# Optimization experiments

Measured on AMD Instinct MI355X. Metric: run time of the kernel, lower is better.

Reference implementation:

```python
import jax, jax.numpy as jnp
import numpy as np

N_NODES = 100000


def gcn_conv(x, edge_index, W, b):
    """PyG-style GCNConv: symmetric-normalized A+I propagation of x @ W, plus bias."""
    n = x.shape[0]
    src, dst = edge_index[0], edge_index[1]
    loops = jnp.arange(n, dtype=src.dtype)
    src = jnp.concatenate([src, loops])  # add self loops
    dst = jnp.concatenate([dst, loops])
    deg = jax.ops.segment_sum(jnp.ones_like(src, dtype=x.dtype), dst, num_segments=n)
    dinv = jnp.where(deg > 0, jax.lax.rsqrt(deg), 0.0)
    norm = dinv[src] * dinv[dst]  # [E+n]
    h = x @ W  # [n, out]
    msg = h[src] * norm[:, None]  # gather + scale
    out = jax.ops.segment_sum(msg, dst, num_segments=n)  # scatter-add
    return out + b


def setup_inputs() -> dict:
    key = jax.random.key(0)
    ks = jax.random.split(key, 5)
    x = jax.random.normal(ks[0], (N_NODES, 4), dtype=jnp.float32)
    edge_index = jax.random.randint(ks[1], (2, 3200000), 0, N_NODES, dtype=jnp.int64)
    W1 = jax.random.normal(ks[2], (4, 64), dtype=jnp.float32) * 0.5
    b1 = jnp.zeros((64,), dtype=jnp.float32)
    W2 = jax.random.normal(ks[3], (64, 32), dtype=jnp.float32) * 0.125
    b2 = jnp.zeros((32,), dtype=jnp.float32)
    return {"x": x, "edge_index": edge_index, "W1": W1, "b1": b1, "W2": W2, "b2": b2}


def reference(x, edge_index, W1, b1, W2, b2):
    h = gcn_conv(x, edge_index, W1, b1)
    h = jax.nn.relu(h)
    # F.dropout with training=False is identity (eval-mode reference)
    h = gcn_conv(h, edge_index, W2, b2)
    return jnp.mean(h, axis=0)  # [32]
```

## Files before the change

### kernel.cpp

```cpp
#include <hip/hip_runtime.h>

#define ST 512
#define EPB 8192
#define HT 1024
#define FT 1024
#define S_LOG 8
#define S 256
#define CAP 8912
#define MAXB 512

__device__ __forceinline__ void gAtomAdd(float* p, float v) {
    unsafeAtomicAdd(p, v);
}

__global__ void k_init(int* __restrict__ cur_d, int* __restrict__ cur_s,
                       float* __restrict__ g, int nb) {
    int t = threadIdx.x;
    if (t < nb) { cur_d[t] = t * CAP; cur_s[t] = t * CAP; }
    if (t < 64) g[t] = 0.0f;
}

__global__ void __launch_bounds__(ST) k_sctr2(
        const int4* __restrict__ src4, const int4* __restrict__ dst4, int E,
        int* __restrict__ cur_d, int* __restrict__ cur_s,
        unsigned* __restrict__ rec_d, unsigned* __restrict__ rec_s, int nb) {
    __shared__ unsigned lrec[EPB];
    __shared__ unsigned short lbkt[EPB];
    __shared__ int cnt[MAXB];
    __shared__ int lst[MAXB];
    __shared__ int gb[MAXB];
    __shared__ int wsum[8];
    int t = threadIdx.x;
    int lane = t & 63, wv = t >> 6;
    int E4 = E >> 2;
    int b4 = blockIdx.x * (EPB / 4);
    int m = min(EPB, E - blockIdx.x * EPB);

    int4 dk[4], sk[4];
    bool v[4];
    #pragma unroll
    for (int k = 0; k < 4; ++k) {
        int idx = b4 + k * ST + t;
        v[k] = idx < E4;
        if (v[k]) { dk[k] = dst4[idx]; sk[k] = src4[idx]; }
    }

    for (int ph = 0; ph < 2; ++ph) {
        int* cursor = ph ? cur_s : cur_d;
        unsigned* rec = ph ? rec_s : rec_d;
        cnt[t] = 0;
        __syncthreads();
        int rk[16];
        #pragma unroll
        for (int k = 0; k < 4; ++k) {
            if (v[k]) {
                int4 K = ph ? sk[k] : dk[k];
                rk[4 * k + 0] = atomicAdd(&cnt[K.x >> S_LOG], 1);
                rk[4 * k + 1] = atomicAdd(&cnt[K.y >> S_LOG], 1);
                rk[4 * k + 2] = atomicAdd(&cnt[K.z >> S_LOG], 1);
                rk[4 * k + 3] = atomicAdd(&cnt[K.w >> S_LOG], 1);
            }
        }
        __syncthreads();
        int c = cnt[t];
        int ic = c;
        #pragma unroll
        for (int o = 1; o < 64; o <<= 1) {
            int u = __shfl_up(ic, o);
            if (lane >= o) ic += u;
        }
        if (lane == 63) wsum[wv] = ic;
        __syncthreads();
        int pre = 0;
        #pragma unroll
        for (int k = 0; k < 7; ++k) pre += (k < wv) ? wsum[k] : 0;
        ic += pre;
        lst[t] = ic - c;
        gb[t] = (c > 0) ? atomicAdd(&cursor[t], c) : 0;
        __syncthreads();
        #pragma unroll
        for (int k = 0; k < 4; ++k) {
            if (v[k]) {
                int4 K = ph ? sk[k] : dk[k];
                int4 P = ph ? dk[k] : sk[k];
                int bb, p;
                bb = K.x >> S_LOG; p = lst[bb] + rk[4 * k + 0];
                lrec[p] = ((unsigned)P.x << S_LOG) | (unsigned)(K.x & (S - 1));
                lbkt[p] = (unsigned short)bb;
                bb = K.y >> S_LOG; p = lst[bb] + rk[4 * k + 1];
                lrec[p] = ((unsigned)P.y << S_LOG) | (unsigned)(K.y & (S - 1));
                lbkt[p] = (unsigned short)bb;
                bb = K.z >> S_LOG; p = lst[bb] + rk[4 * k + 2];
                lrec[p] = ((unsigned)P.z << S_LOG) | (unsigned)(K.z & (S - 1));
                lbkt[p] = (unsigned short)bb;
                bb = K.w >> S_LOG; p = lst[bb] + rk[4 * k + 3];
                lrec[p] = ((unsigned)P.w << S_LOG) | (unsigned)(K.w & (S - 1));
                lbkt[p] = (unsigned short)bb;
            }
        }
        __syncthreads();
        for (int i = t; i < m; i += ST) {
            int bb = lbkt[i];
            rec[gb[bb] + (i - lst[bb])] = lrec[i];
        }
        __syncthreads();
    }
}

__global__ void __launch_bounds__(HT) k_hist(
        const unsigned* __restrict__ rec_d, const int* __restrict__ cur_d,
        const float4* __restrict__ x, float* __restrict__ dinv,
        float4* __restrict__ y, int n) {
    __shared__ int cnt[S];
    int b = blockIdx.x, t = threadIdx.x;
    if (t < S) cnt[t] = 0;
    __syncthreads();
    int lo = b * CAP;
    int m = cur_d[b] - lo;
    int m4 = m >> 2;
    const uint4* rec4 = (const uint4*)(rec_d + lo);
    for (int i = t; i < m4; i += HT) {
        uint4 r = rec4[i];
        atomicAdd(&cnt[r.x & (S - 1)], 1);
        atomicAdd(&cnt[r.y & (S - 1)], 1);
        atomicAdd(&cnt[r.z & (S - 1)], 1);
        atomicAdd(&cnt[r.w & (S - 1)], 1);
    }
    for (int i = (m4 << 2) + t; i < m; i += HT)
        atomicAdd(&cnt[rec_d[lo + i] & (S - 1)], 1);
    __syncthreads();
    int nd = (b << S_LOG) + t;
    if (t < S && nd < n) {
        float dv = rsqrtf((float)cnt[t] + 1.0f);
        dinv[nd] = dv;
        float4 xi = x[nd];
        y[nd] = make_float4(dv * xi.x, dv * xi.y, dv * xi.z, dv * xi.w);
    }
}

__global__ void __launch_bounds__(FT) k_fuse(
        const unsigned* __restrict__ rec_d, const unsigned* __restrict__ rec_s,
        const int* __restrict__ cur_d, const int* __restrict__ cur_s,
        const float4* __restrict__ y, const float* __restrict__ dinv,
        const float* __restrict__ W1, const float* __restrict__ b1,
        float* __restrict__ g, int n) {
    __shared__ unsigned lrec[CAP];
    __shared__ int cnt[S];
    __shared__ int nst[S];
    __shared__ float a[S];
    __shared__ float4 lp1[S];
    __shared__ float red[FT];
    __shared__ int wsum[4];
    int b = blockIdx.x, t = threadIdx.x;
    int lane = t & 63, wv = t >> 6;
    if (t < S) { cnt[t] = 0; a[t] = 0.0f; }
    __syncthreads();
    int lo = b * CAP;
    int md = cur_d[b] - lo;
    unsigned rv[9]; int rr[9];
    #pragma unroll
    for (int k = 0; k < 9; ++k) {
        int i = t + k * FT;
        if (i < md) {
            unsigned r = rec_d[lo + i];
            rv[k] = r;
            rr[k] = atomicAdd(&cnt[r & (S - 1)], 1);
        }
    }
    __syncthreads();
    int c = 0, ic = 0;
    if (t < S) {
        c = cnt[t]; ic = c;
        #pragma unroll
        for (int o = 1; o < 64; o <<= 1) {
            int u = __shfl_up(ic, o);
            if (lane >= o) ic += u;
        }
        if (lane == 63) wsum[wv] = ic;
    }
    __syncthreads();
    if (t < S) {
        int pre = 0;
        #pragma unroll
        for (int k = 0; k < 3; ++k) pre += (k < wv) ? wsum[k] : 0;
        ic += pre;
        cnt[t] = ic;
        nst[t] = ic - c;
    }
    __syncthreads();
    #pragma unroll
    for (int k = 0; k < 9; ++k) {
        int i = t + k * FT;
        if (i < md) lrec[nst[rv[k] & (S - 1)] + rr[k]] = rv[k] >> S_LOG;
    }
    int ms = cur_s[b] - lo;
    int ms4 = ms >> 2;
    const uint4* rs4 = (const uint4*)(rec_s + lo);
    for (int i = t; i < ms4; i += FT) {
        uint4 r = rs4[i];
        float d0 = dinv[r.x >> S_LOG], d1 = dinv[r.y >> S_LOG];
        float d2 = dinv[r.z >> S_LOG], d3 = dinv[r.w >> S_LOG];
        atomicAdd(&a[r.x & (S - 1)], d0);
        atomicAdd(&a[r.y & (S - 1)], d1);
        atomicAdd(&a[r.z & (S - 1)], d2);
        atomicAdd(&a[r.w & (S - 1)], d3);
    }
    for (int i = (ms4 << 2) + t; i < ms; i += FT) {
        unsigned r = rec_s[lo + i];
        atomicAdd(&a[r & (S - 1)], dinv[r >> S_LOG]);
    }
    __syncthreads();
    int node = t >> 2, q = t & 3;
    int nd = (b << S_LOG) + node;
    if (nd < n) {
        int j1 = cnt[node];
        int j = nst[node] + q;
        float a0 = 0.0f, a1 = 0.0f, a2 = 0.0f, a3 = 0.0f;
        for (; j + 12 < j1; j += 16) {
            int s0 = lrec[j], s1 = lrec[j + 4], s2 = lrec[j + 8], s3 = lrec[j + 12];
            float4 y0 = y[s0], y1 = y[s1], y2 = y[s2], y3 = y[s3];
            a0 += y0.x + y1.x + y2.x + y3.x;
            a1 += y0.y + y1.y + y2.y + y3.y;
            a2 += y0.z + y1.z + y2.z + y3.z;
            a3 += y0.w + y1.w + y2.w + y3.w;
        }
        for (; j < j1; j += 4) {
            float4 ys = y[lrec[j]];
            a0 += ys.x; a1 += ys.y; a2 += ys.z; a3 += ys.w;
        }
        a0 += __shfl_down(a0, 2); a1 += __shfl_down(a1, 2);
        a2 += __shfl_down(a2, 2); a3 += __shfl_down(a3, 2);
        a0 += __shfl_down(a0, 1); a1 += __shfl_down(a1, 1);
        a2 += __shfl_down(a2, 1); a3 += __shfl_down(a3, 1);
        if (q == 0) {
            float di = dinv[nd];
            lp1[node] = make_float4(di * a0, di * a1, di * a2, di * a3);
        }
    }
    __syncthreads();
    int cch = t & 63, w = t >> 6;
    float w0 = W1[cch], w1 = W1[64 + cch], w2 = W1[128 + cch], w3 = W1[192 + cch];
    float bb = b1[cch];
    int nb0 = b << S_LOG;
    float facc = 0.0f;
    for (int k = w; k < S; k += 16) {
        int ndk = nb0 + k;
        if (ndk >= n) break;
        float di = dinv[ndk];
        float4 p = lp1[k];
        float4 yi = y[ndk];
        float h0 = fmaf(di, yi.x, p.x);
        float h1 = fmaf(di, yi.y, p.y);
        float h2 = fmaf(di, yi.z, p.z);
        float h3 = fmaf(di, yi.w, p.w);
        float h = fmaf(h0, w0, fmaf(h1, w1, fmaf(h2, w2, fmaf(h3, w3, bb))));
        h = fmaxf(h, 0.0f);
        float wi = fmaf(di, a[k], di * di);
        facc = fmaf(wi, h, facc);
    }
    red[t] = facc;
    __syncthreads();
    if (t < 64) {
        float s = red[t];
        #pragma unroll
        for (int o = 1; o < 16; ++o) s += red[t + 64 * o];
        gAtomAdd(&g[t], s);
    }
}

__global__ void k_final(const float* __restrict__ g, const float* __restrict__ W2,
                        const float* __restrict__ b2, float* __restrict__ out, float inv_n) {
    int j = threadIdx.x;
    if (j < 32) {
        float a = 0.0f;
        #pragma unroll
        for (int c = 0; c < 64; ++c) a = fmaf(g[c], W2[c * 32 + j], a);
        out[j] = fmaf(a, inv_n, b2[j]);
    }
}

extern "C" void kernel_launch(void* const* d_in, const int* in_sizes, int n_in,
                              void* d_out, int out_size, void* d_ws, size_t ws_size,
                              hipStream_t stream) {
    const float* x  = (const float*)d_in[0];
    const int*   ei = (const int*)d_in[1];
    const float* W1 = (const float*)d_in[2];
    const float* b1 = (const float*)d_in[3];
    const float* W2 = (const float*)d_in[4];
    const float* b2 = (const float*)d_in[5];
    float* out = (float*)d_out;

    int n = in_sizes[0] / 4;
    int E = in_sizes[1] / 2;
    const int* src = ei;
    const int* dst = ei + E;
    int NB = (n + S - 1) >> S_LOG;

    char* ws = (char*)d_ws;
    int* cur_d = (int*)ws;
    int* cur_s = cur_d + 512;
    float* g   = (float*)(cur_s + 512);
    size_t ctrl = 1600;
    unsigned* rec_d = (unsigned*)ws + ctrl;
    unsigned* rec_s = rec_d + (size_t)NB * CAP;
    float* y    = (float*)(rec_s + (size_t)NB * CAP);
    float* dinv = y + 4 * (size_t)n;

    int NSB = (E + EPB - 1) / EPB;

    k_init<<<1, 512, 0, stream>>>(cur_d, cur_s, g, NB);
    k_sctr2<<<NSB, ST, 0, stream>>>((const int4*)src, (const int4*)dst, E,
                                    cur_d, cur_s, rec_d, rec_s, NB);
    k_hist<<<NB, HT, 0, stream>>>(rec_d, cur_d, (const float4*)x, dinv,
                                  (float4*)y, n);
    k_fuse<<<NB, FT, 0, stream>>>(rec_d, rec_s, cur_d, cur_s,
                                  (const float4*)y, dinv, W1, b1, g, n);
    k_final<<<1, 64, 0, stream>>>(g, W2, b2, out, 1.0f / (float)n);
}
```

Measured before the change: 148.7 us.

## Drop source-bucketed scatter; compute per-source dinv sums via global atomics

Edges were previously bucketed twice, once by destination and once by source. Now only the destination bucketing remains, and the per-source sum of dinv[dst] is accumulated with global float atomics inside the gather kernel. The fused kernel is split into a gather kernel that writes z per node and a node kernel that applies W1, relu and the weighted reduction, because the atomics must finish across all blocks first. This saves one scatter pass and a record array of writes and reads. It adds about 3.2M random global atomics, an extra z round trip and one more launch.

```diff
diff --git a/kernel.cpp b/kernel.cpp
--- a/kernel.cpp
+++ b/kernel.cpp
@@ -3,7 +3,8 @@
 #define ST 512
 #define EPB 8192
 #define HT 1024
-#define FT 1024
+#define GT 1024
+#define NT 1024
 #define S_LOG 8
 #define S 256
 #define CAP 8912
@@ -13,17 +14,15 @@
     unsafeAtomicAdd(p, v);
 }
 
-__global__ void k_init(int* __restrict__ cur_d, int* __restrict__ cur_s,
-                       float* __restrict__ g, int nb) {
+__global__ void k_init(int* __restrict__ cur_d, float* __restrict__ g, int nb) {
     int t = threadIdx.x;
-    if (t < nb) { cur_d[t] = t * CAP; cur_s[t] = t * CAP; }
+    if (t < nb) cur_d[t] = t * CAP;
     if (t < 64) g[t] = 0.0f;
 }
 
-__global__ void __launch_bounds__(ST) k_sctr2(
+__global__ void __launch_bounds__(ST) k_sctr1(
         const int4* __restrict__ src4, const int4* __restrict__ dst4, int E,
-        int* __restrict__ cur_d, int* __restrict__ cur_s,
-        unsigned* __restrict__ rec_d, unsigned* __restrict__ rec_s, int nb) {
+        int* __restrict__ cur_d, unsigned* __restrict__ rec_d, int nb) {
     __shared__ unsigned lrec[EPB];
     __shared__ unsigned short lbkt[EPB];
     __shared__ int cnt[MAXB];
@@ -45,72 +44,66 @@
         if (v[k]) { dk[k] = dst4[idx]; sk[k] = src4[idx]; }
     }
 
-    for (int ph = 0; ph < 2; ++ph) {
-        int* cursor = ph ? cur_s : cur_d;
-        unsigned* rec = ph ? rec_s : rec_d;
-        cnt[t] = 0;
-        __syncthreads();
-        int rk[16];
-        #pragma unroll
-        for (int k = 0; k < 4; ++k) {
-            if (v[k]) {
-                int4 K = ph ? sk[k] : dk[k];
-                rk[4 * k + 0] = atomicAdd(&cnt[K.x >> S_LOG], 1);
-                rk[4 * k + 1] = atomicAdd(&cnt[K.y >> S_LOG], 1);
-                rk[4 * k + 2] = atomicAdd(&cnt[K.z >> S_LOG], 1);
-                rk[4 * k + 3] = atomicAdd(&cnt[K.w >> S_LOG], 1);
-            }
-        }
-        __syncthreads();
-        int c = cnt[t];
-        int ic = c;
-        #pragma unroll
-        for (int o = 1; o < 64; o <<= 1) {
-            int u = __shfl_up(ic, o);
-            if (lane >= o) ic += u;
-        }
-        if (lane == 63) wsum[wv] = ic;
-        __syncthreads();
-        int pre = 0;
-        #pragma unroll
-        for (int k = 0; k < 7; ++k) pre += (k < wv) ? wsum[k] : 0;
-        ic += pre;
-        lst[t] = ic - c;
-        gb[t] = (c > 0) ? atomicAdd(&cursor[t], c) : 0;
-        __syncthreads();
-        #pragma unroll
-        for (int k = 0; k < 4; ++k) {
-            if (v[k]) {
-                int4 K = ph ? sk[k] : dk[k];
-                int4 P = ph ? dk[k] : sk[k];
-                int bb, p;
-                bb = K.x >> S_LOG; p = lst[bb] + rk[4 * k + 0];
-                lrec[p] = ((unsigned)P.x << S_LOG) | (unsigned)(K.x & (S - 1));
-                lbkt[p] = (unsigned short)bb;
-                bb = K.y >> S_LOG; p = lst[bb] + rk[4 * k + 1];
-                lrec[p] = ((unsigned)P.y << S_LOG) | (unsigned)(K.y & (S - 1));
-                lbkt[p] = (unsigned short)bb;
-                bb = K.z >> S_LOG; p = lst[bb] + rk[4 * k + 2];
-                lrec[p] = ((unsigned)P.z << S_LOG) | (unsigned)(K.z & (S - 1));
-                lbkt[p] = (unsigned short)bb;
-                bb = K.w >> S_LOG; p = lst[bb] + rk[4 * k + 3];
-                lrec[p] = ((unsigned)P.w << S_LOG) | (unsigned)(K.w & (S - 1));
-                lbkt[p] = (unsigned short)bb;
-            }
-        }
-        __syncthreads();
-        for (int i = t; i < m; i += ST) {
-            int bb = lbkt[i];
-            rec[gb[bb] + (i - lst[bb])] = lrec[i];
-        }
-        __syncthreads();
+    cnt[t] = 0;
+    __syncthreads();
+    int rk[16];
+    #pragma unroll
+    for (int k = 0; k < 4; ++k) {
+        if (v[k]) {
+            rk[4 * k + 0] = atomicAdd(&cnt[dk[k].x >> S_LOG], 1);
+            rk[4 * k + 1] = atomicAdd(&cnt[dk[k].y >> S_LOG], 1);
+            rk[4 * k + 2] = atomicAdd(&cnt[dk[k].z >> S_LOG], 1);
+            rk[4 * k + 3] = atomicAdd(&cnt[dk[k].w >> S_LOG], 1);
+        }
+    }
+    __syncthreads();
+    int c = cnt[t];
+    int ic = c;
+    #pragma unroll
+    for (int o = 1; o < 64; o <<= 1) {
+        int u = __shfl_up(ic, o);
+        if (lane >= o) ic += u;
+    }
+    if (lane == 63) wsum[wv] = ic;
+    __syncthreads();
+    int pre = 0;
+    #pragma unroll
+    for (int k = 0; k < 7; ++k) pre += (k < wv) ? wsum[k] : 0;
+    ic += pre;
+    lst[t] = ic - c;
+    gb[t] = (c > 0) ? atomicAdd(&cur_d[t], c) : 0;
+    __syncthreads();
+    #pragma unroll
+    for (int k = 0; k < 4; ++k) {
+        if (v[k]) {
+            int4 K = dk[k];
+            int4 P = sk[k];
+            int bb, p;
+            bb = K.x >> S_LOG; p = lst[bb] + rk[4 * k + 0];
+            lrec[p] = ((unsigned)P.x << S_LOG) | (unsigned)(K.x & (S - 1));
+            lbkt[p] = (unsigned short)bb;
+            bb = K.y >> S_LOG; p = lst[bb] + rk[4 * k + 1];
+            lrec[p] = ((unsigned)P.y << S_LOG) | (unsigned)(K.y & (S - 1));
+            lbkt[p] = (unsigned short)bb;
+            bb = K.z >> S_LOG; p = lst[bb] + rk[4 * k + 2];
+            lrec[p] = ((unsigned)P.z << S_LOG) | (unsigned)(K.z & (S - 1));
+            lbkt[p] = (unsigned short)bb;
+            bb = K.w >> S_LOG; p = lst[bb] + rk[4 * k + 3];
+            lrec[p] = ((unsigned)P.w << S_LOG) | (unsigned)(K.w & (S - 1));
+            lbkt[p] = (unsigned short)bb;
+        }
+    }
+    __syncthreads();
+    for (int i = t; i < m; i += ST) {
+        int bb = lbkt[i];
+        rec_d[gb[bb] + (i - lst[bb])] = lrec[i];
     }
 }
 
 __global__ void __launch_bounds__(HT) k_hist(
         const unsigned* __restrict__ rec_d, const int* __restrict__ cur_d,
         const float4* __restrict__ x, float* __restrict__ dinv,
-        float4* __restrict__ y, int n) {
+        float4* __restrict__ y, float* __restrict__ sumd, int n) {
     __shared__ int cnt[S];
     int b = blockIdx.x, t = threadIdx.x;
     if (t < S) cnt[t] = 0;
@@ -135,36 +128,38 @@
         dinv[nd] = dv;
         float4 xi = x[nd];
         y[nd] = make_float4(dv * xi.x, dv * xi.y, dv * xi.z, dv * xi.w);
-    }
-}
-
-__global__ void __launch_bounds__(FT) k_fuse(
-        const unsigned* __restrict__ rec_d, const unsigned* __restrict__ rec_s,
-        const int* __restrict__ cur_d, const int* __restrict__ cur_s,
+        sumd[nd] = 0.0f;
+    }
+}
+
+__global__ void __launch_bounds__(GT) k_gathz(
+        const unsigned* __restrict__ rec_d, const int* __restrict__ cur_d,
         const float4* __restrict__ y, const float* __restrict__ dinv,
-        const float* __restrict__ W1, const float* __restrict__ b1,
-        float* __restrict__ g, int n) {
+        float* __restrict__ sumd, float4* __restrict__ z, int n) {
     __shared__ unsigned lrec[CAP];
     __shared__ int cnt[S];
     __shared__ int nst[S];
-    __shared__ float a[S];
-    __shared__ float4 lp1[S];
-    __shared__ float red[FT];
+    __shared__ float s_dinv[S];
     __shared__ int wsum[4];
     int b = blockIdx.x, t = threadIdx.x;
     int lane = t & 63, wv = t >> 6;
-    if (t < S) { cnt[t] = 0; a[t] = 0.0f; }
+    if (t < S) {
+        cnt[t] = 0;
+        int nd0 = (b << S_LOG) + t;
+        s_dinv[t] = (nd0 < n) ? dinv[nd0] : 0.0f;
+    }
     __syncthreads();
     int lo = b * CAP;
     int md = cur_d[b] - lo;
     unsigned rv[9]; int rr[9];
     #pragma unroll
     for (int k = 0; k < 9; ++k) {
-        int i = t + k * FT;
+        int i = t + k * GT;
         if (i < md) {
             unsigned r = rec_d[lo + i];
             rv[k] = r;
             rr[k] = atomicAdd(&cnt[r & (S - 1)], 1);
+            gAtomAdd(&sumd[r >> S_LOG], s_dinv[r & (S - 1)]);
         }
     }
     __syncthreads();
@@ -190,24 +185,8 @@
     __syncthreads();
     #pragma unroll
     for (int k = 0; k < 9; ++k) {
-        int i = t + k * FT;
+        int i = t + k * GT;
         if (i < md) lrec[nst[rv[k] & (S - 1)] + rr[k]] = rv[k] >> S_LOG;
-    }
-    int ms = cur_s[b] - lo;
-    int ms4 = ms >> 2;
-    const uint4* rs4 = (const uint4*)(rec_s + lo);
-    for (int i = t; i < ms4; i += FT) {
-        uint4 r = rs4[i];
-        float d0 = dinv[r.x >> S_LOG], d1 = dinv[r.y >> S_LOG];
-        float d2 = dinv[r.z >> S_LOG], d3 = dinv[r.w >> S_LOG];
-        atomicAdd(&a[r.x & (S - 1)], d0);
-        atomicAdd(&a[r.y & (S - 1)], d1);
-        atomicAdd(&a[r.z & (S - 1)], d2);
-        atomicAdd(&a[r.w & (S - 1)], d3);
-    }
-    for (int i = (ms4 << 2) + t; i < ms; i += FT) {
-        unsigned r = rec_s[lo + i];
-        atomicAdd(&a[r & (S - 1)], dinv[r >> S_LOG]);
     }
     __syncthreads();
     int node = t >> 2, q = t & 3;
@@ -233,29 +212,34 @@
         a0 += __shfl_down(a0, 1); a1 += __shfl_down(a1, 1);
         a2 += __shfl_down(a2, 1); a3 += __shfl_down(a3, 1);
         if (q == 0) {
-            float di = dinv[nd];
-            lp1[node] = make_float4(di * a0, di * a1, di * a2, di * a3);
-        }
-    }
-    __syncthreads();
-    int cch = t & 63, w = t >> 6;
-    float w0 = W1[cch], w1 = W1[64 + cch], w2 = W1[128 + cch], w3 = W1[192 + cch];
-    float bb = b1[cch];
+            float di = s_dinv[node];
+            float4 yi = y[nd];
+            z[nd] = make_float4(di * (a0 + yi.x), di * (a1 + yi.y),
+                                di * (a2 + yi.z), di * (a3 + yi.w));
+        }
+    }
+}
+
+__global__ void __launch_bounds__(NT) k_node(
+        const float4* __restrict__ z, const float* __restrict__ dinv,
+        const float* __restrict__ sumd,
+        const float* __restrict__ W1, const float* __restrict__ b1,
+        float* __restrict__ g, int n) {
+    __shared__ float red[NT];
+    int b = blockIdx.x, t = threadIdx.x;
+    int c = t & 63, w = t >> 6;
+    float w0 = W1[c], w1 = W1[64 + c], w2 = W1[128 + c], w3 = W1[192 + c];
+    float bb = b1[c];
     int nb0 = b << S_LOG;
     float facc = 0.0f;
     for (int k = w; k < S; k += 16) {
-        int ndk = nb0 + k;
-        if (ndk >= n) break;
-        float di = dinv[ndk];
-        float4 p = lp1[k];
-        float4 yi = y[ndk];
-        float h0 = fmaf(di, yi.x, p.x);
-        float h1 = fmaf(di, yi.y, p.y);
-        float h2 = fmaf(di, yi.z, p.z);
-        float h3 = fmaf(di, yi.w, p.w);
-        float h = fmaf(h0, w0, fmaf(h1, w1, fmaf(h2, w2, fmaf(h3, w3, bb))));
+        int nd = nb0 + k;
+        if (nd >= n) break;
+        float4 zi = z[nd];
+        float h = fmaf(zi.x, w0, fmaf(zi.y, w1, fmaf(zi.z, w2, fmaf(zi.w, w3, bb))));
         h = fmaxf(h, 0.0f);
-        float wi = fmaf(di, a[k], di * di);
+        float di = dinv[nd];
+        float wi = fmaf(di, sumd[nd], di * di);
         facc = fmaf(wi, h, facc);
     }
     red[t] = facc;
@@ -298,22 +282,23 @@
 
     char* ws = (char*)d_ws;
     int* cur_d = (int*)ws;
-    int* cur_s = cur_d + 512;
-    float* g   = (float*)(cur_s + 512);
+    float* g   = (float*)(cur_d + 512);
     size_t ctrl = 1600;
     unsigned* rec_d = (unsigned*)ws + ctrl;
-    unsigned* rec_s = rec_d + (size_t)NB * CAP;
-    float* y    = (float*)(rec_s + (size_t)NB * CAP);
+    float* y    = (float*)(rec_d + (size_t)NB * CAP);
     float* dinv = y + 4 * (size_t)n;
+    float* sumd = dinv + (size_t)n;
+    float* z    = sumd + (size_t)n;
 
     int NSB = (E + EPB - 1) / EPB;
 
-    k_init<<<1, 512, 0, stream>>>(cur_d, cur_s, g, NB);
-    k_sctr2<<<NSB, ST, 0, stream>>>((const int4*)src, (const int4*)dst, E,
-                                    cur_d, cur_s, rec_d, rec_s, NB);
+    k_init<<<1, 512, 0, stream>>>(cur_d, g, NB);
+    k_sctr1<<<NSB, ST, 0, stream>>>((const int4*)src, (const int4*)dst, E,
+                                    cur_d, rec_d, NB);
     k_hist<<<NB, HT, 0, stream>>>(rec_d, cur_d, (const float4*)x, dinv,
-                                  (float4*)y, n);
-    k_fuse<<<NB, FT, 0, stream>>>(rec_d, rec_s, cur_d, cur_s,
-                                  (const float4*)y, dinv, W1, b1, g, n);
+                                  (float4*)y, sumd, n);
+    k_gathz<<<NB, GT, 0, stream>>>(rec_d, cur_d, (const float4*)y, dinv,
+                                   sumd, (float4*)z, n);
+    k_node<<<NB, NT, 0, stream>>>((const float4*)z, dinv, sumd, W1, b1, g, n);
     k_final<<<1, 64, 0, stream>>>(g, W2, b2, out, 1.0f / (float)n);
 }
```

Result: slower. 285.8 us (+92.2%).

## Vectorize and prefetch bucket record loads in fused kernel; simplify scatter offsets

Applied to the files above, without the earlier changes.

Bucket cursors now start at zero and hold counts, with the CAP base added at scatter time. A per-bucket combined offset replaces two shared lookups in the record write-out. In the fused kernel, the dst records are read as uint4 instead of nine scalar loads, and the src-record loads are issued early into registers so their latency overlaps the counting and prefix-scan phases. This raises register pressure and hardcodes at most three uint4 loads per thread, which matches the CAP capacity.

```diff
diff --git a/kernel.cpp b/kernel.cpp
--- a/kernel.cpp
+++ b/kernel.cpp
@@ -16,7 +16,7 @@
 __global__ void k_init(int* __restrict__ cur_d, int* __restrict__ cur_s,
                        float* __restrict__ g, int nb) {
     int t = threadIdx.x;
-    if (t < nb) { cur_d[t] = t * CAP; cur_s[t] = t * CAP; }
+    if (t < nb) { cur_d[t] = 0; cur_s[t] = 0; }
     if (t < 64) g[t] = 0.0f;
 }
 
@@ -28,7 +28,7 @@
     __shared__ unsigned short lbkt[EPB];
     __shared__ int cnt[MAXB];
     __shared__ int lst[MAXB];
-    __shared__ int gb[MAXB];
+    __shared__ int goff[MAXB];
     __shared__ int wsum[8];
     int t = threadIdx.x;
     int lane = t & 63, wv = t >> 6;
@@ -75,8 +75,10 @@
         #pragma unroll
         for (int k = 0; k < 7; ++k) pre += (k < wv) ? wsum[k] : 0;
         ic += pre;
-        lst[t] = ic - c;
-        gb[t] = (c > 0) ? atomicAdd(&cursor[t], c) : 0;
+        int st = ic - c;
+        lst[t] = st;
+        int gbase = (c > 0) ? t * CAP + atomicAdd(&cursor[t], c) : 0;
+        goff[t] = gbase - st;
         __syncthreads();
         #pragma unroll
         for (int k = 0; k < 4; ++k) {
@@ -100,8 +102,7 @@
         }
         __syncthreads();
         for (int i = t; i < m; i += ST) {
-            int bb = lbkt[i];
-            rec[gb[bb] + (i - lst[bb])] = lrec[i];
+            rec[goff[lbkt[i]] + i] = lrec[i];
         }
         __syncthreads();
     }
@@ -116,7 +117,7 @@
     if (t < S) cnt[t] = 0;
     __syncthreads();
     int lo = b * CAP;
-    int m = cur_d[b] - lo;
+    int m = cur_d[b];
     int m4 = m >> 2;
     const uint4* rec4 = (const uint4*)(rec_d + lo);
     for (int i = t; i < m4; i += HT) {
@@ -154,18 +155,40 @@
     int b = blockIdx.x, t = threadIdx.x;
     int lane = t & 63, wv = t >> 6;
     if (t < S) { cnt[t] = 0; a[t] = 0.0f; }
-    __syncthreads();
     int lo = b * CAP;
-    int md = cur_d[b] - lo;
-    unsigned rv[9]; int rr[9];
-    #pragma unroll
-    for (int k = 0; k < 9; ++k) {
+    int md = cur_d[b];
+    int ms = cur_s[b];
+    const uint4* rs4 = (const uint4*)(rec_s + lo);
+    int ms4 = ms >> 2;
+    uint4 pf[3]; bool pv[3];
+    #pragma unroll
+    for (int k = 0; k < 3; ++k) {
         int i = t + k * FT;
-        if (i < md) {
-            unsigned r = rec_d[lo + i];
-            rv[k] = r;
-            rr[k] = atomicAdd(&cnt[r & (S - 1)], 1);
-        }
+        pv[k] = i < ms4;
+        if (pv[k]) pf[k] = rs4[i];
+    }
+    __syncthreads();
+    const uint4* rd4 = (const uint4*)(rec_d + lo);
+    int md4 = md >> 2;
+    uint4 rv4[3]; int rr4[12]; bool v4[3];
+    #pragma unroll
+    for (int k = 0; k < 3; ++k) {
+        int i = t + k * FT;
+        v4[k] = i < md4;
+        if (v4[k]) {
+            uint4 r = rd4[i];
+            rv4[k] = r;
+            rr4[4 * k + 0] = atomicAdd(&cnt[r.x & (S - 1)], 1);
+            rr4[4 * k + 1] = atomicAdd(&cnt[r.y & (S - 1)], 1);
+            rr4[4 * k + 2] = atomicAdd(&cnt[r.z & (S - 1)], 1);
+            rr4[4 * k + 3] = atomicAdd(&cnt[r.w & (S - 1)], 1);
+        }
+    }
+    unsigned rvt = 0; int rrt = 0;
+    bool vt = t < (md & 3);
+    if (vt) {
+        rvt = rec_d[lo + (md4 << 2) + t];
+        rrt = atomicAdd(&cnt[rvt & (S - 1)], 1);
     }
     __syncthreads();
     int c = 0, ic = 0;
@@ -189,21 +212,27 @@
     }
     __syncthreads();
     #pragma unroll
-    for (int k = 0; k < 9; ++k) {
-        int i = t + k * FT;
-        if (i < md) lrec[nst[rv[k] & (S - 1)] + rr[k]] = rv[k] >> S_LOG;
-    }
-    int ms = cur_s[b] - lo;
-    int ms4 = ms >> 2;
-    const uint4* rs4 = (const uint4*)(rec_s + lo);
-    for (int i = t; i < ms4; i += FT) {
-        uint4 r = rs4[i];
-        float d0 = dinv[r.x >> S_LOG], d1 = dinv[r.y >> S_LOG];
-        float d2 = dinv[r.z >> S_LOG], d3 = dinv[r.w >> S_LOG];
-        atomicAdd(&a[r.x & (S - 1)], d0);
-        atomicAdd(&a[r.y & (S - 1)], d1);
-        atomicAdd(&a[r.z & (S - 1)], d2);
-        atomicAdd(&a[r.w & (S - 1)], d3);
+    for (int k = 0; k < 3; ++k) {
+        if (v4[k]) {
+            uint4 r = rv4[k];
+            lrec[nst[r.x & (S - 1)] + rr4[4 * k + 0]] = r.x >> S_LOG;
+            lrec[nst[r.y & (S - 1)] + rr4[4 * k + 1]] = r.y >> S_LOG;
+            lrec[nst[r.z & (S - 1)] + rr4[4 * k + 2]] = r.z >> S_LOG;
+            lrec[nst[r.w & (S - 1)] + rr4[4 * k + 3]] = r.w >> S_LOG;
+        }
+    }
+    if (vt) lrec[nst[rvt & (S - 1)] + rrt] = rvt >> S_LOG;
+    #pragma unroll
+    for (int k = 0; k < 3; ++k) {
+        if (pv[k]) {
+            uint4 r = pf[k];
+            float d0 = dinv[r.x >> S_LOG], d1 = dinv[r.y >> S_LOG];
+            float d2 = dinv[r.z >> S_LOG], d3 = dinv[r.w >> S_LOG];
+            atomicAdd(&a[r.x & (S - 1)], d0);
+            atomicAdd(&a[r.y & (S - 1)], d1);
+            atomicAdd(&a[r.z & (S - 1)], d2);
+            atomicAdd(&a[r.w & (S - 1)], d3);
+        }
     }
     for (int i = (ms4 << 2) + t; i < ms; i += FT) {
         unsigned r = rec_s[lo + i];
```

Measured after the change: 155.8 us. 1.05x slower.

## Shrink node buckets to 196 nodes via magic-multiply bucketing for more blocks

Applied to the files above, without the earlier changes.

Replaces power-of-two 256-node buckets with 196-node buckets computed by a magic-number multiply-high, raising the bucket count from 391 to about 511. Per-bucket capacity, edges per scatter block and per-thread register arrays shrink to match. The aim is more blocks on the CU-heavy GPU and smaller per-block LDS footprint, so occupancy and load balance improve. It adds a multiply-high per key and ties correctness to the magic constant, the fixed node count and bucket capacity not overflowing (MAXB 512 limit is near).

```diff
diff --git a/kernel.cpp b/kernel.cpp
--- a/kernel.cpp
+++ b/kernel.cpp
@@ -1,16 +1,22 @@
 #include <hip/hip_runtime.h>
 
 #define ST 512
-#define EPB 8192
+#define EPB 6400
 #define HT 1024
 #define FT 1024
 #define S_LOG 8
 #define S 256
-#define CAP 8912
+#define SN 196
+#define MAGIC 21913099u
+#define CAP 6912
 #define MAXB 512
 
 __device__ __forceinline__ void gAtomAdd(float* p, float v) {
     unsafeAtomicAdd(p, v);
+}
+
+__device__ __forceinline__ int bkt(int key) {
+    return (int)__umulhi((unsigned)key, MAGIC);
 }
 
 __global__ void k_init(int* __restrict__ cur_d, int* __restrict__ cur_s,
@@ -33,15 +39,17 @@
     int t = threadIdx.x;
     int lane = t & 63, wv = t >> 6;
     int E4 = E >> 2;
+    int m = min(EPB, E - blockIdx.x * EPB);
+    int m4 = m >> 2;
     int b4 = blockIdx.x * (EPB / 4);
-    int m = min(EPB, E - blockIdx.x * EPB);
 
     int4 dk[4], sk[4];
     bool v[4];
     #pragma unroll
     for (int k = 0; k < 4; ++k) {
-        int idx = b4 + k * ST + t;
-        v[k] = idx < E4;
+        int li = k * ST + t;
+        int idx = b4 + li;
+        v[k] = (li < m4) && (idx < E4);
         if (v[k]) { dk[k] = dst4[idx]; sk[k] = src4[idx]; }
     }
 
@@ -55,10 +63,10 @@
         for (int k = 0; k < 4; ++k) {
             if (v[k]) {
                 int4 K = ph ? sk[k] : dk[k];
-                rk[4 * k + 0] = atomicAdd(&cnt[K.x >> S_LOG], 1);
-                rk[4 * k + 1] = atomicAdd(&cnt[K.y >> S_LOG], 1);
-                rk[4 * k + 2] = atomicAdd(&cnt[K.z >> S_LOG], 1);
-                rk[4 * k + 3] = atomicAdd(&cnt[K.w >> S_LOG], 1);
+                rk[4 * k + 0] = atomicAdd(&cnt[bkt(K.x)], 1);
+                rk[4 * k + 1] = atomicAdd(&cnt[bkt(K.y)], 1);
+                rk[4 * k + 2] = atomicAdd(&cnt[bkt(K.z)], 1);
+                rk[4 * k + 3] = atomicAdd(&cnt[bkt(K.w)], 1);
             }
         }
         __syncthreads();
@@ -84,17 +92,17 @@
                 int4 K = ph ? sk[k] : dk[k];
                 int4 P = ph ? dk[k] : sk[k];
                 int bb, p;
-                bb = K.x >> S_LOG; p = lst[bb] + rk[4 * k + 0];
-                lrec[p] = ((unsigned)P.x << S_LOG) | (unsigned)(K.x & (S - 1));
+                bb = bkt(K.x); p = lst[bb] + rk[4 * k + 0];
+                lrec[p] = ((unsigned)P.x << S_LOG) | (unsigned)(K.x - bb * SN);
                 lbkt[p] = (unsigned short)bb;
-                bb = K.y >> S_LOG; p = lst[bb] + rk[4 * k + 1];
-                lrec[p] = ((unsigned)P.y << S_LOG) | (unsigned)(K.y & (S - 1));
+                bb = bkt(K.y); p = lst[bb] + rk[4 * k + 1];
+                lrec[p] = ((unsigned)P.y << S_LOG) | (unsigned)(K.y - bb * SN);
                 lbkt[p] = (unsigned short)bb;
-                bb = K.z >> S_LOG; p = lst[bb] + rk[4 * k + 2];
-                lrec[p] = ((unsigned)P.z << S_LOG) | (unsigned)(K.z & (S - 1));
+                bb = bkt(K.z); p = lst[bb] + rk[4 * k + 2];
+                lrec[p] = ((unsigned)P.z << S_LOG) | (unsigned)(K.z - bb * SN);
                 lbkt[p] = (unsigned short)bb;
-                bb = K.w >> S_LOG; p = lst[bb] + rk[4 * k + 3];
-                lrec[p] = ((unsigned)P.w << S_LOG) | (unsigned)(K.w & (S - 1));
+                bb = bkt(K.w); p = lst[bb] + rk[4 * k + 3];
+                lrec[p] = ((unsigned)P.w << S_LOG) | (unsigned)(K.w - bb * SN);
                 lbkt[p] = (unsigned short)bb;
             }
         }
@@ -129,8 +137,8 @@
     for (int i = (m4 << 2) + t; i < m; i += HT)
         atomicAdd(&cnt[rec_d[lo + i] & (S - 1)], 1);
     __syncthreads();
-    int nd = (b << S_LOG) + t;
-    if (t < S && nd < n) {
+    int nd = b * SN + t;
+    if (t < SN && nd < n) {
         float dv = rsqrtf((float)cnt[t] + 1.0f);
         dinv[nd] = dv;
         float4 xi = x[nd];
@@ -157,9 +165,9 @@
     __syncthreads();
     int lo = b * CAP;
     int md = cur_d[b] - lo;
-    unsigned rv[9]; int rr[9];
+    unsigned rv[7]; int rr[7];
     #pragma unroll
-    for (int k = 0; k < 9; ++k) {
+    for (int k = 0; k < 7; ++k) {
         int i = t + k * FT;
         if (i < md) {
             unsigned r = rec_d[lo + i];
@@ -189,7 +197,7 @@
     }
     __syncthreads();
     #pragma unroll
-    for (int k = 0; k < 9; ++k) {
+    for (int k = 0; k < 7; ++k) {
         int i = t + k * FT;
         if (i < md) lrec[nst[rv[k] & (S - 1)] + rr[k]] = rv[k] >> S_LOG;
     }
@@ -211,8 +219,8 @@
     }
     __syncthreads();
     int node = t >> 2, q = t & 3;
-    int nd = (b << S_LOG) + node;
-    if (nd < n) {
+    int nd = b * SN + node;
+    if (node < SN && nd < n) {
         int j1 = cnt[node];
         int j = nst[node] + q;
         float a0 = 0.0f, a1 = 0.0f, a2 = 0.0f, a3 = 0.0f;
@@ -241,9 +249,9 @@
     int cch = t & 63, w = t >> 6;
     float w0 = W1[cch], w1 = W1[64 + cch], w2 = W1[128 + cch], w3 = W1[192 + cch];
     float bb = b1[cch];
-    int nb0 = b << S_LOG;
+    int nb0 = b * SN;
     float facc = 0.0f;
-    for (int k = w; k < S; k += 16) {
+    for (int k = w; k < SN; k += 16) {
         int ndk = nb0 + k;
         if (ndk >= n) break;
         float di = dinv[ndk];
@@ -294,7 +302,7 @@
     int E = in_sizes[1] / 2;
     const int* src = ei;
     const int* dst = ei + E;
-    int NB = (n + S - 1) >> S_LOG;
+    int NB = (n + SN - 1) / SN;
 
     char* ws = (char*)d_ws;
     int* cur_d = (int*)ws;
```

New measurement: 153.1 us. 3.0% more time.
